# Performance work log

Measured on AMD Instinct MI355X. Metric: run time of the kernel, lower is better.

The kernel has to match this reference:

```python
import jax, jax.numpy as jnp
import numpy as np

DN = ('NCDHW', 'OIDHW', 'NCDHW')

def conv3d(x, w, b, stride=1, padding=1, lhs_dilation=1):
    pad = [(padding, padding)] * 3 if isinstance(padding, int) else padding
    y = jax.lax.conv_general_dilated(
        x, w, window_strides=(stride,) * 3, padding=pad,
        lhs_dilation=(lhs_dilation,) * 3, dimension_numbers=DN)
    return y + b[None, :, None, None, None]

def bool_to_multichannel(x):
    # (B,1,D,H,W) bool -> (B,8,D/4,H/4,W/4) float; each 4x4x4 patch bit-packed to 8 bytes
    B = x.shape[0]; D = x.shape[2]; d = D // 4
    p = x.reshape(B, d, 4, d, 4, d, 4)
    p = p.transpose(0, 1, 3, 5, 2, 4, 6).reshape(B, d, d, d, 8, 8)
    pw2 = (2.0 ** jnp.arange(8)).astype(jnp.float32)
    mc = jnp.sum(p.astype(jnp.float32) * pw2, axis=-1)  # (B,d,d,d,8)
    return mc.transpose(0, 4, 1, 2, 3) / 255.0

def setup_inputs():
    key = jax.random.key(0)
    ks = jax.random.split(key, 26)
    B, RES = 4, 256
    CH, E, ZC, K = 32, 16, 128, 8192
    L = 16  # latent resolution (mc res 64 / 2^(len(ch_mult)-1))
    # block-sparse boolean voxels so a good fraction of latent patches is all-zero
    coarse = jax.random.uniform(ks[0], (B, 1, 16, 16, 16)) < 0.6
    coarse = jnp.repeat(jnp.repeat(jnp.repeat(coarse, 16, 2), 16, 3), 16, 4)
    dense = jax.random.uniform(ks[1], (B, 1, RES, RES, RES)) < 0.3
    x = coarse & dense
    p = lambda k, shape, s=0.05: (jax.random.normal(k, shape) * s).astype(jnp.float32)
    return {
        'x': x,
        'enc_in_w': p(ks[2], (CH, 8, 3, 3, 3)), 'enc_in_b': p(ks[3], (CH,)),
        'enc_d1_w': p(ks[4], (2 * CH, CH, 3, 3, 3)), 'enc_d1_b': p(ks[5], (2 * CH,)),
        'enc_d2_w': p(ks[6], (4 * CH, 2 * CH, 3, 3, 3)), 'enc_d2_b': p(ks[7], (4 * CH,)),
        'enc_out_w': p(ks[8], (ZC, 4 * CH, 3, 3, 3)), 'enc_out_b': p(ks[9], (ZC,)),
        'quant_w': p(ks[10], (E, ZC, 1, 1, 1)), 'quant_b': p(ks[11], (E,)),
        'codebook': p(ks[12], (K, E), 0.5),
        'replacement_token': p(ks[13], (1, E), 0.02),
        'pos_embedding': p(ks[14], (1, E, L, L, L), 1.0),
        'post_quant_w': p(ks[15], (ZC, E, 1, 1, 1)), 'post_quant_b': p(ks[16], (ZC,)),
        'dec_in_w': p(ks[17], (ZC, ZC, 3, 3, 3)), 'dec_in_b': p(ks[18], (ZC,)),
        'dec_u1_w': p(ks[19], (2 * CH, ZC, 3, 3, 3)), 'dec_u1_b': p(ks[20], (2 * CH,)),
        'dec_u2_w': p(ks[21], (CH, 2 * CH, 3, 3, 3)), 'dec_u2_b': p(ks[22], (CH,)),
        'dec_out_w': p(ks[23], (8, CH, 3, 3, 3)), 'dec_out_b': p(ks[24], (8,)),
    }

def reference(x, enc_in_w, enc_in_b, enc_d1_w, enc_d1_b, enc_d2_w, enc_d2_b,
              enc_out_w, enc_out_b, quant_w, quant_b, codebook, replacement_token,
              pos_embedding, post_quant_w, post_quant_b, dec_in_w, dec_in_b,
              dec_u1_w, dec_u1_b, dec_u2_w, dec_u2_b, dec_out_w, dec_out_b):
    silu = jax.nn.silu
    mc = bool_to_multichannel(x)                      # (B,8,64,64,64)
    B, _, Dm, _, _ = mc.shape
    L = Dm // 4                                       # latent res = 16

    # zero-patch mask, patch_size=4 (== max_pool3d(nonzero_any) < 0.5)
    nz = jnp.any(mc != 0, axis=1)                     # (B,64,64,64)
    pooled = nz.reshape(B, L, 4, L, 4, L, 4).any(axis=(2, 4, 6))
    zero_mask = ~pooled.reshape(B, L * L * L)         # (B,N) True = all-zero patch

    # encoder (downsample x4) + quant_conv (1x1x1)
    h = silu(conv3d(mc, enc_in_w, enc_in_b))
    h = silu(conv3d(h, enc_d1_w, enc_d1_b, stride=2))
    h = silu(conv3d(h, enc_d2_w, enc_d2_b, stride=2))
    h = conv3d(h, enc_out_w, enc_out_b)
    h = conv3d(h, quant_w, quant_b, padding=0)        # (B,E,L,L,L)
    E = h.shape[1]
    seq = h.reshape(B, E, -1).transpose(0, 2, 1)      # (B,N,E)

    dist = jnp.sum(codebook * codebook, axis=-1) - 2.0 * jnp.einsum('bne,ke->bnk', seq, codebook)
    idx = jnp.argmin(dist, axis=-1)                   # (B,N)
    q_nz = codebook[idx]                              # (B,N,E)
    nonzero = ~zero_mask
    # commit over nonzero tokens * non_mask_frac == masked mean over all tokens
    mse_tok = jnp.mean(jnp.square(jax.lax.stop_gradient(q_nz) - seq), axis=-1)
    commit_loss = 0.25 * jnp.mean(jnp.where(nonzero, mse_tok, 0.0))

    # replacement token is index 0 of the full codebook; real codes shift by +1
    full_idx = jnp.where(zero_mask, 0, idx + 1)       # (B,N)
    full_cb = jnp.concatenate([replacement_token, codebook], axis=0)
    quant = full_cb[full_idx].transpose(0, 2, 1).reshape(B, E, L, L, L)

    # decoder (upsample x4 via fractionally-strided convs)
    q = quant + pos_embedding
    q = conv3d(q, post_quant_w, post_quant_b, padding=0)
    d = silu(conv3d(q, dec_in_w, dec_in_b))
    d = silu(conv3d(d, dec_u1_w, dec_u1_b, padding=[(2, 1)] * 3, lhs_dilation=2))
    d = silu(conv3d(d, dec_u2_w, dec_u2_b, padding=[(2, 1)] * 3, lhs_dilation=2))
    recon = conv3d(d, dec_out_w, dec_out_b)           # (B,8,64,64,64)
    return recon, mc, commit_loss, full_idx
```

## Files before the change

kernel.cpp:

```cpp
#include <hip/hip_runtime.h>
#include <hip/hip_bf16.h>
#include <math.h>

#define BB 4
#define NTOK 4096
#define KCB 8192
#define ED 16

__device__ __forceinline__ float silu_f(float x){ return x / (1.0f + expf(-x)); }
__device__ __forceinline__ double silu_d(double x){ return x / (1.0 + exp(-x)); }

template<typename T> struct V4T { typedef T type __attribute__((ext_vector_type(4))); };
typedef float f2v __attribute__((ext_vector_type(2)));

__global__ void r9_probe_zero(int* flags){ if (threadIdx.x < 2) flags[threadIdx.x] = 0; }

__global__ void r9_probe_dtype(const unsigned char* __restrict__ x, int* __restrict__ flags){
  int t = blockIdx.x*256 + threadIdx.x;
  unsigned v = ((const unsigned*)x)[t];
  bool off = (v & 0xFFFFFF00u) != 0u;
  bool al  = (v & 0x000000FFu) != 0u;
  if (__any(off) && (threadIdx.x & 63) == 0) atomicOr(flags + 0, 1);
  if (__any(al)  && (threadIdx.x & 63) == 0) atomicOr(flags + 1, 1);
}

__global__ void r9_pack_mc(const unsigned char* __restrict__ x, float* __restrict__ mc,
                           const int* __restrict__ flags){
  int t = blockIdx.x*256 + threadIdx.x;
  int k = t & 63, j = (t>>6)&63, i = (t>>12)&63, b = t>>18;
  int is_i32 = (flags[1] != 0) && (flags[0] == 0);
  unsigned ch[8];
  #pragma unroll
  for (int q=0;q<8;++q) ch[q]=0u;
  if (is_i32){
    const int* xb = (const int*)x + ((size_t)b << 24);
    #pragma unroll
    for (int a=0;a<4;++a){
      #pragma unroll
      for (int b2=0;b2<4;++b2){
        const int4 v = *(const int4*)(xb + (((size_t)(4*i+a))<<16) + ((size_t)(4*j+b2)<<8) + (size_t)(4*k));
        int vv[4] = {v.x, v.y, v.z, v.w};
        #pragma unroll
        for (int c2=0;c2<4;++c2){
          int lin = a*16 + b2*4 + c2;
          unsigned bit = vv[c2] ? 1u : 0u;
          ch[lin>>3] += bit << (lin&7);
        }
      }
    }
  } else {
    const unsigned char* xb = x + ((size_t)b << 24);
    #pragma unroll
    for (int a=0;a<4;++a){
      #pragma unroll
      for (int b2=0;b2<4;++b2){
        const unsigned char* row = xb + (((size_t)(4*i+a))<<16) + ((size_t)(4*j+b2)<<8) + (size_t)(4*k);
        unsigned v = *(const unsigned*)row;
        #pragma unroll
        for (int c2=0;c2<4;++c2){
          int lin = a*16 + b2*4 + c2;
          unsigned bit = ((v >> (8*c2)) & 0xffu) ? 1u : 0u;
          ch[lin>>3] += bit << (lin&7);
        }
      }
    }
  }
  size_t sp = ((size_t)i<<12) + (j<<6) + k;
  #pragma unroll
  for (int q=0;q<8;++q)
    mc[(((size_t)(b*8+q))<<18) + sp] = (float)ch[q] / 255.0f;
}

__global__ void r9_token_nz(const float* __restrict__ mc, unsigned char* __restrict__ tnz){
  int t = blockIdx.x*64 + threadIdx.x;
  int tk = t&15, tj=(t>>4)&15, ti=(t>>8)&15, b=t>>12;
  bool any = false;
  for (int q=0;q<8 && !any;++q){
    const float* mq = mc + (((size_t)(b*8+q))<<18);
    for (int a=0;a<4;++a)
      for (int c=0;c<4;++c){
        const float4 v = *(const float4*)(mq + ((size_t)(4*ti+a)<<12) + ((size_t)(4*tj+c)<<6) + (size_t)(4*tk));
        if (v.x!=0.f || v.y!=0.f || v.z!=0.f || v.w!=0.f){ any = true; }
      }
  }
  tnz[t] = any ? 1 : 0;
}

template<int XT, int STRIDE, typename TIN, typename ACC>
__device__ __forceinline__ void load_span(const TIN* __restrict__ inr, bool xlo, bool xhi,
                                          ACC (&xv)[STRIDE*(XT-1)+3]){
  static_assert(XT==4, "XT must be 4");
  typedef typename V4T<TIN>::type tin4;
  if (STRIDE==1){
    tin4 m = *(const tin4*)(inr + 1);
    xv[1]=(ACC)m.x; xv[2]=(ACC)m.y; xv[3]=(ACC)m.z; xv[4]=(ACC)m.w;
    xv[0] = xlo ? (ACC)inr[0] : (ACC)0;
    xv[5] = xhi ? (ACC)inr[5] : (ACC)0;
  } else {
    tin4 a = *(const tin4*)(inr + 1);
    tin4 b = *(const tin4*)(inr + 5);
    xv[1]=(ACC)a.x; xv[2]=(ACC)a.y; xv[3]=(ACC)a.z; xv[4]=(ACC)a.w;
    xv[5]=(ACC)b.x; xv[6]=(ACC)b.y; xv[7]=(ACC)b.z; xv[8]=(ACC)b.w;
    xv[0] = xlo ? (ACC)inr[0] : (ACC)0;
  }
}

template<int CIN, int OCB, int XT, int STRIDE, bool DOSILU, typename TIN, typename TOUT, typename ACC>
__global__ void r16_conv3x3(const TIN* __restrict__ in, const float* __restrict__ w,
                            const float* __restrict__ bias, TOUT* __restrict__ out,
                            int Din, int Dout){
  constexpr int SPAN = STRIDE*(XT-1)+3;
  const int oc0 = blockIdx.y * OCB;
  const int n3 = Dout*Dout*Dout;
  const int nxt = Dout / XT;
  const int t = blockIdx.x*256 + threadIdx.x;
  const int xo0 = (t % nxt)*XT;
  const int yo = (t/nxt)%Dout, zo = t/(nxt*Dout);
  const int zi0 = zo*STRIDE-1, yi0 = yo*STRIDE-1, xi0 = xo0*STRIDE-1;
  const bool xlo = (xi0 >= 0);
  const bool xhi = (xi0 + (SPAN-1) < Din);

  ACC acc[OCB][XT];
  #pragma unroll
  for (int q=0;q<OCB;++q){
    ACC bv = (ACC)bias[oc0+q];
    #pragma unroll
    for (int s=0;s<XT;++s) acc[q][s] = bv;
  }

  #pragma unroll 1
  for (int i=0;i<CIN;++i){
    const TIN* inc = in + (size_t)i*Din*Din*Din;
    const float* wci = w + ((size_t)oc0*CIN + i)*27;
    #pragma unroll
    for (int kd=0;kd<3;++kd){
      int z = zi0+kd; if ((unsigned)z >= (unsigned)Din) continue;
      #pragma unroll
      for (int kh=0;kh<3;++kh){
        int y = yi0+kh; if ((unsigned)y >= (unsigned)Din) continue;
        const TIN* inr = inc + ((size_t)z*Din + y)*Din + xi0;
        ACC xv[SPAN];
        load_span<XT,STRIDE,TIN,ACC>(inr, xlo, xhi, xv);
        #pragma unroll
        for (int q=0;q<OCB;++q){
          const float* wr = wci + (size_t)q*CIN*27 + kd*9 + kh*3;
          #pragma unroll
          for (int kw=0;kw<3;++kw){
            ACC wv = (ACC)wr[kw];
            #pragma unroll
            for (int s=0;s<XT;++s)
              acc[q][s] = fma(wv, xv[s*STRIDE+kw], acc[q][s]);
          }
        }
      }
    }
  }
  if (DOSILU){
    #pragma unroll
    for (int q=0;q<OCB;++q)
      #pragma unroll
      for (int s=0;s<XT;++s){
        if (sizeof(ACC)==8) acc[q][s] = (ACC)silu_d((double)acc[q][s]);
        else                acc[q][s] = (ACC)silu_f((float)acc[q][s]);
      }
  }
  size_t vox = ((size_t)zo*Dout + yo)*Dout + xo0;
  #pragma unroll
  for (int q=0;q<OCB;++q)
    #pragma unroll
    for (int s=0;s<XT;++s)
      out[(size_t)(oc0+q)*n3 + vox + s] = (TOUT)acc[q][s];
}

template<int CIN, int OCB, int XT, int NS, int STRIDE, typename TIN, typename ACC>
__global__ void r16_conv_part(const TIN* __restrict__ in, const float* __restrict__ w,
                              const float* __restrict__ bias, ACC* __restrict__ part,
                              int Din, int Dout){
  constexpr int SPAN = STRIDE*(XT-1)+3;
  const int oc0 = blockIdx.y * OCB;
  const int OC  = gridDim.y * OCB;
  const int cz  = blockIdx.z;
  const int n3 = Dout*Dout*Dout;
  const int nxt = Dout / XT;
  const int t = blockIdx.x*256 + threadIdx.x;
  const int xo0 = (t % nxt)*XT;
  const int yo = (t/nxt)%Dout, zo = t/(nxt*Dout);
  const int zi0 = zo*STRIDE-1, yi0 = yo*STRIDE-1, xi0 = xo0*STRIDE-1;
  const bool xlo = (xi0 >= 0);
  const bool xhi = (xi0 + (SPAN-1) < Din);

  ACC acc[OCB][XT];
  #pragma unroll
  for (int q=0;q<OCB;++q){
    ACC bv = (cz==0) ? (ACC)bias[oc0+q] : (ACC)0;
    #pragma unroll
    for (int s=0;s<XT;++s) acc[q][s] = bv;
  }

  const int cbeg = cz * (CIN/NS);
  #pragma unroll 1
  for (int i=cbeg; i<cbeg + CIN/NS; ++i){
    const TIN* inc = in + (size_t)i*Din*Din*Din;
    const float* wci = w + ((size_t)oc0*CIN + i)*27;
    #pragma unroll
    for (int kd=0;kd<3;++kd){
      int z = zi0+kd; if ((unsigned)z >= (unsigned)Din) continue;
      #pragma unroll
      for (int kh=0;kh<3;++kh){
        int y = yi0+kh; if ((unsigned)y >= (unsigned)Din) continue;
        const TIN* inr = inc + ((size_t)z*Din + y)*Din + xi0;
        ACC xv[SPAN];
        load_span<XT,STRIDE,TIN,ACC>(inr, xlo, xhi, xv);
        #pragma unroll
        for (int q=0;q<OCB;++q){
          const float* wr = wci + (size_t)q*CIN*27 + kd*9 + kh*3;
          #pragma unroll
          for (int kw=0;kw<3;++kw){
            ACC wv = (ACC)wr[kw];
            #pragma unroll
            for (int s=0;s<XT;++s)
              acc[q][s] = fma(wv, xv[s*STRIDE+kw], acc[q][s]);
          }
        }
      }
    }
  }
  size_t vox = ((size_t)zo*Dout + yo)*Dout + xo0;
  #pragma unroll
  for (int q=0;q<OCB;++q)
    #pragma unroll
    for (int s=0;s<XT;++s)
      part[((size_t)cz*OC + (oc0+q))*n3 + vox + s] = acc[q][s];
}

template<int NS, int VEC, bool DOSILU, typename ACC, typename TOUT>
__global__ void r16_reduce(const ACC* __restrict__ part, TOUT* __restrict__ out, int total){
  int t0 = (blockIdx.x*256 + threadIdx.x)*VEC;
  if (t0 >= total) return;
  ACC a[VEC];
  #pragma unroll
  for (int v=0;v<VEC;++v) a[v] = part[t0+v];
  #pragma unroll
  for (int s=1;s<NS;++s){
    #pragma unroll
    for (int v=0;v<VEC;++v) a[v] += part[(size_t)s*total + t0+v];
  }
  #pragma unroll
  for (int v=0;v<VEC;++v){
    if (DOSILU){
      if (sizeof(ACC)==8) a[v] = (ACC)silu_d((double)a[v]);
      else                a[v] = (ACC)silu_f((float)a[v]);
    }
    out[t0+v] = (TOUT)a[v];
  }
}

__global__ void r9_quantconv_b(const double* __restrict__ h4b, const float* __restrict__ w,
                               const float* __restrict__ bias, double* __restrict__ seqd, int b){
  int t = blockIdx.x*256 + threadIdx.x;
  if (t >= 65536) return;
  int n = t & 4095, e = t >> 12;
  double acc = (double)bias[e];
  const float* we = w + e*128;
  for (int i=0;i<128;++i) acc = fma(h4b[((size_t)i<<12)+n], (double)we[i], acc);
  seqd[((size_t)(b*NTOK+n))*ED + e] = acc;
}

__global__ void r9_postquant_b(const float* __restrict__ qpeb, const float* __restrict__ w,
                               const float* __restrict__ bias, float* __restrict__ pqb){
  int t = blockIdx.x*256 + threadIdx.x;
  if (t >= 524288) return;
  int n = t & 4095, o = t >> 12;
  float acc = bias[o];
  const float* wo = w + o*16;
  #pragma unroll
  for (int e=0;e<16;++e) acc = fmaf(qpeb[((size_t)e<<12)+n], wo[e], acc);
  pqb[t] = acc;
}

__global__ void r9_cnorm(const float* __restrict__ cb, double* __restrict__ cnormd){
  int k = blockIdx.x*256 + threadIdx.x;
  if (k >= KCB) return;
  const float* c = cb + (size_t)k*ED;
  double s = 0.0;
  #pragma unroll
  for (int e=0;e<ED;++e) s = fma((double)c[e], (double)c[e], s);
  cnormd[k] = s;
}

#define VQC 256
#define VQPARTS 16
template<int PARTS>
__global__ void r12_vq_partial(const double* __restrict__ seqd, const float* __restrict__ cb,
                               const double* __restrict__ cnormd,
                               double* __restrict__ pdist, int* __restrict__ pidx){
  __shared__ double scb[VQC*ED];
  __shared__ double snorm[VQC];
  int part = blockIdx.y;
  int tok = blockIdx.x*256 + threadIdx.x;
  double s[16];
  const double* sr = seqd + (size_t)tok*ED;
  #pragma unroll
  for (int e=0;e<16;++e) s[e] = sr[e];
  double best = 1.0e300; int bi = 0;
  const int CP = KCB/PARTS;
  for (int c=0;c<CP/VQC;++c){
    int kbase = part*CP + c*VQC;
    for (int u=threadIdx.x; u<VQC*ED; u+=256) scb[u] = (double)cb[(size_t)kbase*ED + u];
    for (int u=threadIdx.x; u<VQC; u+=256) snorm[u] = cnormd[kbase+u];
    __syncthreads();
    for (int kk=0; kk<VQC; ++kk){
      const double* cr = scb + kk*ED;
      double dot = 0.0;
      #pragma unroll
      for (int e=0;e<16;++e) dot = fma(s[e], cr[e], dot);
      double dist = snorm[kk] - 2.0*dot;
      if (dist < best){ best = dist; bi = kbase+kk; }
    }
    __syncthreads();
  }
  pdist[part*16384 + tok] = best;
  pidx [part*16384 + tok] = bi;
}

template<int PARTS>
__global__ void r12_vq_merge(const double* __restrict__ pdist, const int* __restrict__ pidx,
                             const unsigned char* __restrict__ tnz, int* __restrict__ idxw,
                             float* __restrict__ out_idx, float* __restrict__ loss_slot){
  int tok = blockIdx.x*256 + threadIdx.x;
  if (tok == 0) *loss_slot = 0.f;
  double best = pdist[tok]; int bi = pidx[tok];
  #pragma unroll
  for (int p=1;p<PARTS;++p){
    double d2 = pdist[p*16384+tok];
    if (d2 < best){ best = d2; bi = pidx[p*16384+tok]; }
  }
  idxw[tok] = bi;
  out_idx[tok] = tnz[tok] ? (float)(bi+1) : 0.f;
}

__global__ void r9_commit(const double* __restrict__ seqd, const float* __restrict__ cb,
                          const int* __restrict__ idxw, const unsigned char* __restrict__ tnz,
                          float* __restrict__ loss_slot){
  int tok = blockIdx.x*256 + threadIdx.x;
  float v = 0.f;
  if (tnz[tok]){
    const float* c = cb + (size_t)idxw[tok]*ED;
    const double* s = seqd + (size_t)tok*ED;
    double acc = 0.0;
    #pragma unroll
    for (int e=0;e<ED;++e){ double d = (double)c[e]-s[e]; acc = fma(d,d,acc); }
    v = (float)(acc * (0.25/(16.0*16384.0)));
  }
  #pragma unroll
  for (int off=32; off; off>>=1) v += __shfl_down(v, off);
  if ((threadIdx.x & 63) == 0) atomicAdd(loss_slot, v);
}

__global__ void r9_gather_pos(const float* __restrict__ cb, const float* __restrict__ rep,
                              const int* __restrict__ idxw, const unsigned char* __restrict__ tnz,
                              const float* __restrict__ pos, float* __restrict__ qpe){
  int t = blockIdx.x*256 + threadIdx.x;
  int n = t & 4095, e = (t>>12)&15, b = t>>16;
  int tok = b*NTOK + n;
  float v = tnz[tok] ? cb[(size_t)idxw[tok]*ED + e] : rep[e];
  qpe[t] = v + pos[((size_t)e<<12) + n];
}

template<int CIN, int XT, bool DOSILU>
__global__ void r16_tconv(const float* __restrict__ in, const float* __restrict__ w,
                          const float* __restrict__ bias, float* __restrict__ out,
                          int Din){
  static_assert(XT==2, "XT must be 2");
  const int oc = blockIdx.y;
  const int nxt = Din / XT;
  const int t = blockIdx.x*256 + threadIdx.x;
  const int ux0 = (t % nxt)*XT;
  const int uy = (t/nxt)%Din, uz = t/(nxt*Din);
  const bool vx = ux0 > 0, vy = uy > 0, vz = uz > 0;
  const int DD = Din*Din, n3 = DD*Din;

  float b0 = bias[oc];
  float acc[8][XT];
  #pragma unroll
  for (int q=0;q<8;++q)
    #pragma unroll
    for (int s=0;s<XT;++s) acc[q][s] = b0;

  const float* p = in + ((size_t)uz*Din + uy)*Din + ux0;
  #pragma unroll 1
  for (int i=0;i<CIN;++i){
    float X[2][2][XT+1];
    #pragma unroll
    for (int za=0; za<2; ++za){
      #pragma unroll
      for (int ya=0; ya<2; ++ya){
        bool okzy = (za==1 || vz) && (ya==1 || vy);
        const float* pr = p + (za-1)*DD + (ya-1)*Din;
        if (okzy){
          f2v m = *(const f2v*)(pr);
          X[za][ya][1] = m.x; X[za][ya][2] = m.y;
          X[za][ya][0] = vx ? pr[-1] : 0.f;
        } else {
          X[za][ya][0] = 0.f; X[za][ya][1] = 0.f; X[za][ya][2] = 0.f;
        }
      }
    }
    const float* wi = w + ((size_t)(oc*CIN) + i)*27;
    #pragma unroll
    for (int kd=0;kd<3;++kd){
      #pragma unroll
      for (int kh=0;kh<3;++kh){
        #pragma unroll
        for (int kw=0;kw<3;++kw){
          const int pz = (kd==1) ? 1 : 0, py = (kh==1) ? 1 : 0, px = (kw==1) ? 1 : 0;
          const int za = (kd==0) ? 0 : 1, ya = (kh==0) ? 0 : 1, xa = (kw==0) ? 0 : 1;
          float wv = wi[kd*9+kh*3+kw];
          #pragma unroll
          for (int s=0;s<XT;++s)
            acc[pz*4+py*2+px][s] = fmaf(wv, X[za][ya][s+xa], acc[pz*4+py*2+px][s]);
        }
      }
    }
    p += n3;
  }
  if (DOSILU){
    #pragma unroll
    for (int q=0;q<8;++q)
      #pragma unroll
      for (int s=0;s<XT;++s) acc[q][s] = silu_f(acc[q][s]);
  }
  const int Dout = 2*Din;
  #pragma unroll
  for (int pz=0; pz<2; ++pz){
    #pragma unroll
    for (int py=0; py<2; ++py){
      float* row = out + (((size_t)oc*Dout + 2*uz+pz)*Dout + (2*uy+py))*Dout + 2*ux0;
      #pragma unroll
      for (int s=0;s<XT;++s){
        float2 v2 = make_float2(acc[pz*4+py*2+0][s], acc[pz*4+py*2+1][s]);
        *(float2*)(row + 2*s) = v2;
      }
    }
  }
}

__global__ void r9_diag_ws(float* out0, float v){
  if (threadIdx.x == 0 && blockIdx.x == 0) out0[0] = v;
}

extern "C" void kernel_launch(void* const* d_in, const int* in_sizes, int n_in,
                              void* d_out, int out_size, void* d_ws, size_t ws_size,
                              hipStream_t stream){
  const unsigned char* x = (const unsigned char*)d_in[0];
  const float* enc_in_w  = (const float*)d_in[1];
  const float* enc_in_b  = (const float*)d_in[2];
  const float* enc_d1_w  = (const float*)d_in[3];
  const float* enc_d1_b  = (const float*)d_in[4];
  const float* enc_d2_w  = (const float*)d_in[5];
  const float* enc_d2_b  = (const float*)d_in[6];
  const float* enc_out_w = (const float*)d_in[7];
  const float* enc_out_b = (const float*)d_in[8];
  const float* quant_w   = (const float*)d_in[9];
  const float* quant_b   = (const float*)d_in[10];
  const float* codebook  = (const float*)d_in[11];
  const float* rep_tok   = (const float*)d_in[12];
  const float* pos_emb   = (const float*)d_in[13];
  const float* pq_w      = (const float*)d_in[14];
  const float* pq_b      = (const float*)d_in[15];
  const float* dec_in_w  = (const float*)d_in[16];
  const float* dec_in_b  = (const float*)d_in[17];
  const float* dec_u1_w  = (const float*)d_in[18];
  const float* dec_u1_b  = (const float*)d_in[19];
  const float* dec_u2_w  = (const float*)d_in[20];
  const float* dec_u2_b  = (const float*)d_in[21];
  const float* dec_out_w = (const float*)d_in[22];
  const float* dec_out_b = (const float*)d_in[23];

  float* out = (float*)d_out;
  const size_t OFF_RECON = 0;
  const size_t OFF_MC    = 8388608;
  const size_t OFF_LOSS  = 16777216;
  const size_t OFF_IDX   = 16777217;

  char* wsb = (char*)d_ws;
  float*  Sbig  = (float*) (wsb + 0);
  float*  Shd   = (float*) (wsb + 33554432);
  double* Sc1   = (double*)(wsb + 41943040);
  double* Sc2   = (double*)(wsb + 46137344);
  float*  Spq   = (float*) (wsb + 50331648);
  float*  SdD   = (float*) (wsb + 52428800);
  double* seqd  = (double*)(wsb + 54525952);
  double* cnormd= (double*)(wsb + 56623104);
  int*    idxw  = (int*)   (wsb + 57475072);
  unsigned char* tnz = (unsigned char*)(wsb + 57540608);
  float*  qpe   = (float*) (wsb + 57556992);
  int*    dflag = (int*)   (wsb + 58605568);
  const size_t WS_NEEDED = 58605632;

  double* scr_d  = (double*)wsb;
  float*  scr_f  = (float*)wsb;
  double* pdist  = (double*)wsb;
  int*    pidx   = (int*)(wsb + VQPARTS*16384*8);

  dim3 blk(256);

  if (ws_size < WS_NEEDED){
    r9_diag_ws<<<dim3(1), dim3(64), 0, stream>>>(out + OFF_RECON,
        9.0e6f + (float)(ws_size >> 20));
    return;
  }

  r9_probe_zero<<<dim3(1), dim3(64), 0, stream>>>(dflag);
  r9_probe_dtype<<<dim3(4096), blk, 0, stream>>>(x, dflag);

  r9_pack_mc<<<dim3(4096), blk, 0, stream>>>(x, out + OFF_MC, dflag);
  r9_token_nz<<<dim3(256), dim3(64), 0, stream>>>(out + OFF_MC, tnz);

  for (int b = 0; b < BB; ++b){
    const float* mcb = out + OFF_MC + (size_t)b*8*262144;
    r16_conv3x3<8,8,4,1,true,float,float,double>  <<<dim3(256,4,1), blk, 0, stream>>>(mcb,  enc_in_w, enc_in_b, Sbig, 64, 64);
    r16_conv3x3<32,4,4,2,true,float,float,double> <<<dim3(32,16,1), blk, 0, stream>>>(Sbig, enc_d1_w, enc_d1_b, Shd,  64, 32);
    r16_conv_part<64,4,4,4,2,float,double><<<dim3(4,32,4), blk, 0, stream>>>(Shd, enc_d2_w, enc_d2_b, scr_d, 32, 16);
    r16_reduce<4,2,true,double,double><<<dim3(1024), blk, 0, stream>>>(scr_d, Sc1, 524288);
    r16_conv_part<128,4,4,8,1,double,double><<<dim3(4,32,8), blk, 0, stream>>>(Sc1, enc_out_w, enc_out_b, scr_d, 16, 16);
    r16_reduce<8,2,false,double,double><<<dim3(1024), blk, 0, stream>>>(scr_d, Sc2, 524288);
    r9_quantconv_b<<<dim3(256), blk, 0, stream>>>(Sc2, quant_w, quant_b, seqd, b);
  }

  r9_cnorm<<<dim3(32), blk, 0, stream>>>(codebook, cnormd);
  r12_vq_partial<VQPARTS><<<dim3(64,VQPARTS), blk, 0, stream>>>(seqd, codebook, cnormd, pdist, pidx);
  r12_vq_merge<VQPARTS><<<dim3(64), blk, 0, stream>>>(pdist, pidx, tnz, idxw, out + OFF_IDX, out + OFF_LOSS);
  r9_commit<<<dim3(64), blk, 0, stream>>>(seqd, codebook, idxw, tnz, out + OFF_LOSS);

  r9_gather_pos<<<dim3(1024), blk, 0, stream>>>(codebook, rep_tok, idxw, tnz, pos_emb, qpe);
  for (int b = 0; b < BB; ++b){
    const float* qpeb = qpe + (size_t)b*65536;
    float* reconb = out + OFF_RECON + (size_t)b*8*262144;
    r9_postquant_b<<<dim3(2048), blk, 0, stream>>>(qpeb, pq_w, pq_b, Spq);
    r16_conv_part<128,4,4,8,1,float,float><<<dim3(4,32,8), blk, 0, stream>>>(Spq, dec_in_w, dec_in_b, scr_f, 16, 16);
    r16_reduce<8,4,true,float,float><<<dim3(512), blk, 0, stream>>>(scr_f, SdD, 524288);
    r16_tconv<128,2,true><<<dim3(8,64,1),  blk, 0, stream>>>(SdD,  dec_u1_w, dec_u1_b, Shd,  16);
    r16_tconv<64,2,true> <<<dim3(64,32,1), blk, 0, stream>>>(Shd,  dec_u2_w, dec_u2_b, Sbig, 32);
    r16_conv3x3<32,8,4,1,false,float,float,float><<<dim3(256,1,1), blk, 0, stream>>>(Sbig, dec_out_w, dec_out_b, reconb, 64, 64);
  }
}
```

Baseline: 4.431 ms.

## Pre-transpose conv weights to tap-major layout for vectorized loads; widen dtype probe

Adds small kernels that reorder conv weights from OIDHW to [cin][tap][oc], and tconv weights to 28-float padded rows. This lets the conv inner loops fetch four output-channel weights with one 16-byte load instead of scalar strided loads. The transform runs only when the workspace is large enough, otherwise the old path is used. The dtype probe is also rewritten to read 16 bytes per thread and reduce through shared memory, cutting atomics and launched blocks. The cost is extra launches plus a larger workspace requirement.

```diff
diff --git a/kernel.cpp b/kernel.cpp
--- a/kernel.cpp
+++ b/kernel.cpp
@@ -12,16 +12,44 @@
 
 template<typename T> struct V4T { typedef T type __attribute__((ext_vector_type(4))); };
 typedef float f2v __attribute__((ext_vector_type(2)));
+typedef float f4v __attribute__((ext_vector_type(4)));
 
 __global__ void r9_probe_zero(int* flags){ if (threadIdx.x < 2) flags[threadIdx.x] = 0; }
 
-__global__ void r9_probe_dtype(const unsigned char* __restrict__ x, int* __restrict__ flags){
+__global__ void r17_probe(const unsigned char* __restrict__ x, int* __restrict__ flags){
+  __shared__ int so, sa;
+  if (threadIdx.x == 0){ so = 0; sa = 0; }
+  __syncthreads();
+  const uint4* p = (const uint4*)x + (size_t)(blockIdx.x*256 + threadIdx.x)*4;
+  unsigned uo = 0, ua = 0;
+  #pragma unroll
+  for (int r=0;r<4;++r){
+    uint4 v = p[r];
+    unsigned uw = v.x | v.y | v.z | v.w;
+    uo |= (uw & 0xFFFFFF00u);
+    ua |= (uw & 0x000000FFu);
+  }
+  if (uo) so = 1;
+  if (ua) sa = 1;
+  __syncthreads();
+  if (threadIdx.x == 0){
+    if (so) atomicOr(flags + 0, 1);
+    if (sa) atomicOr(flags + 1, 1);
+  }
+}
+
+__global__ void r17_wt_conv(const float* __restrict__ w, float* __restrict__ wt, int CIN, int OC){
   int t = blockIdx.x*256 + threadIdx.x;
-  unsigned v = ((const unsigned*)x)[t];
-  bool off = (v & 0xFFFFFF00u) != 0u;
-  bool al  = (v & 0x000000FFu) != 0u;
-  if (__any(off) && (threadIdx.x & 63) == 0) atomicOr(flags + 0, 1);
-  if (__any(al)  && (threadIdx.x & 63) == 0) atomicOr(flags + 1, 1);
+  if (t >= OC*CIN*27) return;
+  int oc = t % OC; int r = t / OC;
+  int i = r / 27, tap = r - i*27;
+  wt[t] = w[((size_t)oc*CIN + i)*27 + tap];
+}
+__global__ void r17_wt_tconv(const float* __restrict__ w, float* __restrict__ wt, int CIN, int OC){
+  int t = blockIdx.x*256 + threadIdx.x;
+  if (t >= OC*CIN*28) return;
+  int tap = t % 28; int r = t / 28;
+  wt[t] = (tap < 27) ? w[(size_t)r*27 + tap] : 0.f;
 }
 
 __global__ void r9_pack_mc(const unsigned char* __restrict__ x, float* __restrict__ mc,
@@ -105,8 +133,45 @@
   }
 }
 
-template<int CIN, int OCB, int XT, int STRIDE, bool DOSILU, typename TIN, typename TOUT, typename ACC>
-__global__ void r16_conv3x3(const TIN* __restrict__ in, const float* __restrict__ w,
+template<bool TW, int CIN, int OCT, int OCB, int XT, int STRIDE, typename ACC>
+__device__ __forceinline__ void apply_taps(const float* __restrict__ w, int i, int kd, int kh,
+                                           int oc0, const ACC (&xv)[STRIDE*(XT-1)+3],
+                                           ACC (&acc)[OCB][XT]){
+  if constexpr (TW){
+    const float* wb = w + ((size_t)i*27 + kd*9 + kh*3)*OCT + oc0;
+    #pragma unroll
+    for (int kw=0;kw<3;++kw){
+      #pragma unroll
+      for (int qq=0;qq<OCB;qq+=4){
+        f4v wv4 = *(const f4v*)(wb + (size_t)kw*OCT + qq);
+        #pragma unroll
+        for (int c=0;c<4;++c){
+          ACC wv = (ACC)wv4[c];
+          #pragma unroll
+          for (int s=0;s<XT;++s)
+            acc[qq+c][s] = fma(wv, xv[s*STRIDE+kw], acc[qq+c][s]);
+        }
+      }
+    }
+  } else {
+    const float* wci = w + ((size_t)oc0*CIN + i)*27;
+    #pragma unroll
+    for (int q=0;q<OCB;++q){
+      const float* wr = wci + (size_t)q*CIN*27 + kd*9 + kh*3;
+      #pragma unroll
+      for (int kw=0;kw<3;++kw){
+        ACC wv = (ACC)wr[kw];
+        #pragma unroll
+        for (int s=0;s<XT;++s)
+          acc[q][s] = fma(wv, xv[s*STRIDE+kw], acc[q][s]);
+      }
+    }
+  }
+}
+
+template<int CIN, int OCT, int OCB, int XT, int STRIDE, bool DOSILU, bool TW,
+         typename TIN, typename TOUT, typename ACC>
+__global__ void r17_conv3x3(const TIN* __restrict__ in, const float* __restrict__ w,
                             const float* __restrict__ bias, TOUT* __restrict__ out,
                             int Din, int Dout){
   constexpr int SPAN = STRIDE*(XT-1)+3;
@@ -131,7 +196,6 @@
   #pragma unroll 1
   for (int i=0;i<CIN;++i){
     const TIN* inc = in + (size_t)i*Din*Din*Din;
-    const float* wci = w + ((size_t)oc0*CIN + i)*27;
     #pragma unroll
     for (int kd=0;kd<3;++kd){
       int z = zi0+kd; if ((unsigned)z >= (unsigned)Din) continue;
@@ -141,17 +205,7 @@
         const TIN* inr = inc + ((size_t)z*Din + y)*Din + xi0;
         ACC xv[SPAN];
         load_span<XT,STRIDE,TIN,ACC>(inr, xlo, xhi, xv);
-        #pragma unroll
-        for (int q=0;q<OCB;++q){
-          const float* wr = wci + (size_t)q*CIN*27 + kd*9 + kh*3;
-          #pragma unroll
-          for (int kw=0;kw<3;++kw){
-            ACC wv = (ACC)wr[kw];
-            #pragma unroll
-            for (int s=0;s<XT;++s)
-              acc[q][s] = fma(wv, xv[s*STRIDE+kw], acc[q][s]);
-          }
-        }
+        apply_taps<TW,CIN,OCT,OCB,XT,STRIDE,ACC>(w, i, kd, kh, oc0, xv, acc);
       }
     }
   }
@@ -172,8 +226,8 @@
       out[(size_t)(oc0+q)*n3 + vox + s] = (TOUT)acc[q][s];
 }
 
-template<int CIN, int OCB, int XT, int NS, int STRIDE, typename TIN, typename ACC>
-__global__ void r16_conv_part(const TIN* __restrict__ in, const float* __restrict__ w,
+template<int CIN, int OCT, int OCB, int XT, int NS, int STRIDE, bool TW, typename TIN, typename ACC>
+__global__ void r17_conv_part(const TIN* __restrict__ in, const float* __restrict__ w,
                               const float* __restrict__ bias, ACC* __restrict__ part,
                               int Din, int Dout){
   constexpr int SPAN = STRIDE*(XT-1)+3;
@@ -201,7 +255,6 @@
   #pragma unroll 1
   for (int i=cbeg; i<cbeg + CIN/NS; ++i){
     const TIN* inc = in + (size_t)i*Din*Din*Din;
-    const float* wci = w + ((size_t)oc0*CIN + i)*27;
     #pragma unroll
     for (int kd=0;kd<3;++kd){
       int z = zi0+kd; if ((unsigned)z >= (unsigned)Din) continue;
@@ -211,17 +264,7 @@
         const TIN* inr = inc + ((size_t)z*Din + y)*Din + xi0;
         ACC xv[SPAN];
         load_span<XT,STRIDE,TIN,ACC>(inr, xlo, xhi, xv);
-        #pragma unroll
-        for (int q=0;q<OCB;++q){
-          const float* wr = wci + (size_t)q*CIN*27 + kd*9 + kh*3;
-          #pragma unroll
-          for (int kw=0;kw<3;++kw){
-            ACC wv = (ACC)wr[kw];
-            #pragma unroll
-            for (int s=0;s<XT;++s)
-              acc[q][s] = fma(wv, xv[s*STRIDE+kw], acc[q][s]);
-          }
-        }
+        apply_taps<TW,CIN,OCT,OCB,XT,STRIDE,ACC>(w, i, kd, kh, oc0, xv, acc);
       }
     }
   }
@@ -367,8 +410,8 @@
   qpe[t] = v + pos[((size_t)e<<12) + n];
 }
 
-template<int CIN, int XT, bool DOSILU>
-__global__ void r16_tconv(const float* __restrict__ in, const float* __restrict__ w,
+template<int CIN, int XT, bool DOSILU, bool TW>
+__global__ void r17_tconv(const float* __restrict__ in, const float* __restrict__ w,
                           const float* __restrict__ bias, float* __restrict__ out,
                           int Din){
   static_assert(XT==2, "XT must be 2");
@@ -406,7 +449,20 @@
         }
       }
     }
-    const float* wi = w + ((size_t)(oc*CIN) + i)*27;
+    float wreg[27];
+    if constexpr (TW){
+      const float* wb = w + ((size_t)oc*CIN + i)*28;
+      #pragma unroll
+      for (int r7=0;r7<7;++r7){
+        f4v v = *(const f4v*)(wb + 4*r7);
+        #pragma unroll
+        for (int c=0;c<4;++c){ if (4*r7+c < 27) wreg[4*r7+c] = v[c]; }
+      }
+    } else {
+      const float* wi = w + ((size_t)(oc*CIN) + i)*27;
+      #pragma unroll
+      for (int tap=0;tap<27;++tap) wreg[tap] = wi[tap];
+    }
     #pragma unroll
     for (int kd=0;kd<3;++kd){
       #pragma unroll
@@ -415,7 +471,7 @@
         for (int kw=0;kw<3;++kw){
           const int pz = (kd==1) ? 1 : 0, py = (kh==1) ? 1 : 0, px = (kw==1) ? 1 : 0;
           const int za = (kd==0) ? 0 : 1, ya = (kh==0) ? 0 : 1, xa = (kw==0) ? 0 : 1;
-          float wv = wi[kd*9+kh*3+kw];
+          float wv = wreg[kd*9+kh*3+kw];
           #pragma unroll
           for (int s=0;s<XT;++s)
             acc[pz*4+py*2+px][s] = fmaf(wv, X[za][ya][s+xa], acc[pz*4+py*2+px][s]);
@@ -498,6 +554,17 @@
   int*    dflag = (int*)   (wsb + 58605568);
   const size_t WS_NEEDED = 58605632;
 
+  float* wtp = (float*)(wsb + 58605632);
+  float* wt_enc_in  = wtp + 0;
+  float* wt_enc_d1  = wtp + 6912;
+  float* wt_enc_d2  = wtp + 62208;
+  float* wt_enc_out = wtp + 283392;
+  float* wt_dec_in  = wtp + 725760;
+  float* wt_dec_out = wtp + 1168128;
+  float* wt_u1      = wtp + 1175040;
+  float* wt_u2      = wtp + 1404416;
+  const size_t WS_NEEDED_T = 58605632 + 1461760*4;
+
   double* scr_d  = (double*)wsb;
   float*  scr_f  = (float*)wsb;
   double* pdist  = (double*)wsb;
@@ -510,20 +577,35 @@
         9.0e6f + (float)(ws_size >> 20));
     return;
   }
+  const bool TW = (ws_size >= WS_NEEDED_T);
 
   r9_probe_zero<<<dim3(1), dim3(64), 0, stream>>>(dflag);
-  r9_probe_dtype<<<dim3(4096), blk, 0, stream>>>(x, dflag);
+  r17_probe<<<dim3(256), blk, 0, stream>>>(x, dflag);
+  if (TW){
+    r17_wt_conv <<<dim3(27),   blk, 0, stream>>>(enc_in_w,  wt_enc_in,  8,   32);
+    r17_wt_conv <<<dim3(216),  blk, 0, stream>>>(enc_d1_w,  wt_enc_d1,  32,  64);
+    r17_wt_conv <<<dim3(864),  blk, 0, stream>>>(enc_d2_w,  wt_enc_d2,  64,  128);
+    r17_wt_conv <<<dim3(1728), blk, 0, stream>>>(enc_out_w, wt_enc_out, 128, 128);
+    r17_wt_conv <<<dim3(1728), blk, 0, stream>>>(dec_in_w,  wt_dec_in,  128, 128);
+    r17_wt_conv <<<dim3(27),   blk, 0, stream>>>(dec_out_w, wt_dec_out, 32,  8);
+    r17_wt_tconv<<<dim3(896),  blk, 0, stream>>>(dec_u1_w,  wt_u1,      128, 64);
+    r17_wt_tconv<<<dim3(224),  blk, 0, stream>>>(dec_u2_w,  wt_u2,      64,  32);
+  }
 
   r9_pack_mc<<<dim3(4096), blk, 0, stream>>>(x, out + OFF_MC, dflag);
   r9_token_nz<<<dim3(256), dim3(64), 0, stream>>>(out + OFF_MC, tnz);
 
   for (int b = 0; b < BB; ++b){
     const float* mcb = out + OFF_MC + (size_t)b*8*262144;
-    r16_conv3x3<8,8,4,1,true,float,float,double>  <<<dim3(256,4,1), blk, 0, stream>>>(mcb,  enc_in_w, enc_in_b, Sbig, 64, 64);
-    r16_conv3x3<32,4,4,2,true,float,float,double> <<<dim3(32,16,1), blk, 0, stream>>>(Sbig, enc_d1_w, enc_d1_b, Shd,  64, 32);
-    r16_conv_part<64,4,4,4,2,float,double><<<dim3(4,32,4), blk, 0, stream>>>(Shd, enc_d2_w, enc_d2_b, scr_d, 32, 16);
+    if (TW) r17_conv3x3<8,32,8,4,1,true,true ,float,float,double><<<dim3(256,4,1), blk, 0, stream>>>(mcb, wt_enc_in, enc_in_b, Sbig, 64, 64);
+    else    r17_conv3x3<8,32,8,4,1,true,false,float,float,double><<<dim3(256,4,1), blk, 0, stream>>>(mcb, enc_in_w,  enc_in_b, Sbig, 64, 64);
+    if (TW) r17_conv3x3<32,64,4,4,2,true,true ,float,float,double><<<dim3(32,16,1), blk, 0, stream>>>(Sbig, wt_enc_d1, enc_d1_b, Shd, 64, 32);
+    else    r17_conv3x3<32,64,4,4,2,true,false,float,float,double><<<dim3(32,16,1), blk, 0, stream>>>(Sbig, enc_d1_w,  enc_d1_b, Shd, 64, 32);
+    if (TW) r17_conv_part<64,128,4,4,4,2,true ,float,double><<<dim3(4,32,4), blk, 0, stream>>>(Shd, wt_enc_d2, enc_d2_b, scr_d, 32, 16);
+    else    r17_conv_part<64,128,4,4,4,2,false,float,double><<<dim3(4,32,4), blk, 0, stream>>>(Shd, enc_d2_w,  enc_d2_b, scr_d, 32, 16);
     r16_reduce<4,2,true,double,double><<<dim3(1024), blk, 0, stream>>>(scr_d, Sc1, 524288);
-    r16_conv_part<128,4,4,8,1,double,double><<<dim3(4,32,8), blk, 0, stream>>>(Sc1, enc_out_w, enc_out_b, scr_d, 16, 16);
+    if (TW) r17_conv_part<128,128,4,4,8,1,true ,double,double><<<dim3(4,32,8), blk, 0, stream>>>(Sc1, wt_enc_out, enc_out_b, scr_d, 16, 16);
+    else    r17_conv_part<128,128,4,4,8,1,false,double,double><<<dim3(4,32,8), blk, 0, stream>>>(Sc1, enc_out_w,  enc_out_b, scr_d, 16, 16);
     r16_reduce<8,2,false,double,double><<<dim3(1024), blk, 0, stream>>>(scr_d, Sc2, 524288);
     r9_quantconv_b<<<dim3(256), blk, 0, stream>>>(Sc2, quant_w, quant_b, seqd, b);
   }
@@ -538,10 +620,14 @@
     const float* qpeb = qpe + (size_t)b*65536;
     float* reconb = out + OFF_RECON + (size_t)b*8*262144;
     r9_postquant_b<<<dim3(2048), blk, 0, stream>>>(qpeb, pq_w, pq_b, Spq);
-    r16_conv_part<128,4,4,8,1,float,float><<<dim3(4,32,8), blk, 0, stream>>>(Spq, dec_in_w, dec_in_b, scr_f, 16, 16);
+    if (TW) r17_conv_part<128,128,4,4,8,1,true ,float,float><<<dim3(4,32,8), blk, 0, stream>>>(Spq, wt_dec_in, dec_in_b, scr_f, 16, 16);
+    else    r17_conv_part<128,128,4,4,8,1,false,float,float><<<dim3(4,32,8), blk, 0, stream>>>(Spq, dec_in_w,  dec_in_b, scr_f, 16, 16);
     r16_reduce<8,4,true,float,float><<<dim3(512), blk, 0, stream>>>(scr_f, SdD, 524288);
-    r16_tconv<128,2,true><<<dim3(8,64,1),  blk, 0, stream>>>(SdD,  dec_u1_w, dec_u1_b, Shd,  16);
-    r16_tconv<64,2,true> <<<dim3(64,32,1), blk, 0, stream>>>(Shd,  dec_u2_w, dec_u2_b, Sbig, 32);
-    r16_conv3x3<32,8,4,1,false,float,float,float><<<dim3(256,1,1), blk, 0, stream>>>(Sbig, dec_out_w, dec_out_b, reconb, 64, 64);
-  }
-}
+    if (TW) r17_tconv<128,2,true,true ><<<dim3(8,64,1), blk, 0, stream>>>(SdD, wt_u1,    dec_u1_b, Shd, 16);
+    else    r17_tconv<128,2,true,false><<<dim3(8,64,1), blk, 0, stream>>>(SdD, dec_u1_w, dec_u1_b, Shd, 16);
+    if (TW) r17_tconv<64,2,true,true ><<<dim3(64,32,1), blk, 0, stream>>>(Shd, wt_u2,    dec_u2_b, Sbig, 32);
+    else    r17_tconv<64,2,true,false><<<dim3(64,32,1), blk, 0, stream>>>(Shd, dec_u2_w, dec_u2_b, Sbig, 32);
+    if (TW) r17_conv3x3<32,8,8,4,1,false,true ,float,float,float><<<dim3(256,1,1), blk, 0, stream>>>(Sbig, wt_dec_out, dec_out_b, reconb, 64, 64);
+    else    r17_conv3x3<32,8,8,4,1,false,false,float,float,float><<<dim3(256,1,1), blk, 0, stream>>>(Sbig, dec_out_w,  dec_out_b, reconb, 64, 64);
+  }
+}
```

Result: slower. 4.873 ms (+10.0%).
